# Optimization experiments

Hardware: AMD Instinct MI355X
Metric: run time of the kernel (lower is better)

Reference implementation:

```python
import jax, jax.numpy as jnp
import numpy as np

B, NV, JN = 1024, 8, 21
V = NV * JN            # 168 tokens = num_view * joint_num
F_DIM, NH, DQ, DV = 512, 4, 128, 128
HID = 512
EPS = 1e-6
NEG = float(-2**32 + 1)


def _layer_norm(x, g, b):
    mu = jnp.mean(x, axis=-1, keepdims=True)
    var = jnp.mean(jnp.square(x - mu), axis=-1, keepdims=True)
    return (x - mu) * jax.lax.rsqrt(var + EPS) * g + b


def setup_inputs() -> dict:
    key = jax.random.key(0)
    ks = jax.random.split(key, 12)
    s = 0.02
    return {
        "x": jax.random.normal(ks[0], (B, V, F_DIM), dtype=jnp.float32),
        "valid": jax.random.randint(ks[1], (B, NV), 0, 2),
        "wq": jax.random.normal(ks[2], (NH * DQ, F_DIM), dtype=jnp.float32) * s,
        "bq": jnp.zeros((NH * DQ,), dtype=jnp.float32),
        "wk": jax.random.normal(ks[3], (NH * DQ, F_DIM), dtype=jnp.float32) * s,
        "bk": jnp.zeros((NH * DQ,), dtype=jnp.float32),
        "wv": jax.random.normal(ks[4], (NH * DV, F_DIM), dtype=jnp.float32) * s,
        "bv": jnp.zeros((NH * DV,), dtype=jnp.float32),
        "fc_w": jax.random.normal(ks[5], (F_DIM, NH * DV), dtype=jnp.float32) * s,
        "fc_b": jnp.zeros((F_DIM,), dtype=jnp.float32),
        "ln1_g": jnp.ones((F_DIM,), dtype=jnp.float32),
        "ln1_b": jnp.zeros((F_DIM,), dtype=jnp.float32),
        "ln2_g": jnp.ones((F_DIM,), dtype=jnp.float32),
        "ln2_b": jnp.zeros((F_DIM,), dtype=jnp.float32),
        "fc1_w": jax.random.normal(ks[6], (HID, F_DIM), dtype=jnp.float32) * s,
        "fc1_b": jnp.zeros((HID,), dtype=jnp.float32),
        "fc2_w": jax.random.normal(ks[7], (F_DIM, HID), dtype=jnp.float32) * s,
        "fc2_b": jnp.zeros((F_DIM,), dtype=jnp.float32),
    }


def reference(x, valid, wq, bq, wk, bk, wv, bv, fc_w, fc_b,
              ln1_g, ln1_b, ln2_g, ln2_b, fc1_w, fc1_b, fc2_w, fc2_b):
    bs = x.shape[0]
    h = _layer_norm(x, ln1_g, ln1_b)                          # [B,V,f]
    q = (h @ wq.T + bq).reshape(bs, V, NH, DQ)                # [B,V,H,dq]
    k = (h @ wk.T + bk).reshape(bs, V, NH, DQ)
    v = (h @ wv.T + bv).reshape(bs, V, NH, DV)
    attn = jnp.einsum('bqhd,bkhd->bhqk', q, k) / jnp.sqrt(jnp.float32(DQ))
    # valid mask: per-view validity expanded to per-token, pairwise additive
    w = jnp.where(valid == 0, NEG, 0.0).astype(x.dtype)       # [B,NV]
    w = jnp.repeat(w, JN, axis=1)                             # [B,V], view-major
    m = w[:, :, None] + w[:, None, :]                         # [B,V,V]
    attn = attn + m[:, None, :, :]
    attn = jax.nn.softmax(attn, axis=-1)
    out = jnp.einsum('bhqk,bkhd->bqhd', attn, v).reshape(bs, V, NH * DV)
    out = out @ fc_w.T + fc_b
    x = x + out
    # MLP residual block
    h2 = _layer_norm(x, ln2_g, ln2_b)
    h2 = jax.nn.relu(h2 @ fc1_w.T + fc1_b) @ fc2_w.T + fc2_b
    return x + h2
```

## Files before the change

### kernel.cpp

```cpp
#include <hip/hip_runtime.h>
#include <stdint.h>

#define BATCH 1024
#define NVIEW 8
#define JN_   21
#define VTOK  168
#define FDIM  512
#define NHEAD 4
#define DHEAD 128
#define MROWS (BATCH*VTOK)
#define SCALE2 0.127517434f

typedef __attribute__((ext_vector_type(8))) short s8v;
typedef __attribute__((ext_vector_type(4))) short s4v;
typedef __attribute__((ext_vector_type(4))) float f4v;

static __device__ __forceinline__ short f2bf(float f){
  unsigned u = __builtin_bit_cast(unsigned, f);
  unsigned r = (u + 0x7FFFu + ((u >> 16) & 1u)) >> 16;
  return (short)(unsigned short)r;
}
static __device__ __forceinline__ float bf2f(short s){
  unsigned u = ((unsigned)(unsigned short)s) << 16;
  return __builtin_bit_cast(float, u);
}

#define GL16(gp, lp) __builtin_amdgcn_global_load_lds( \
    (__attribute__((address_space(1))) void*)(gp), \
    (__attribute__((address_space(3))) void*)(lp), 16, 0, 0)

__global__ __launch_bounds__(256) void convert_w(
    const float* __restrict__ wq, const float* __restrict__ wk,
    const float* __restrict__ wv, const float* __restrict__ fcw,
    const float* __restrict__ fc1, const float* __restrict__ fc2,
    short* __restrict__ dst){
  int id = blockIdx.x * 256 + threadIdx.x;
  int e = id * 4;
  int seg = e >> 18;
  int off = e & 262143;
  const float* s = seg==0?wq: seg==1?wk: seg==2?wv: seg==3?fcw: seg==4?fc1: fc2;
  float4 u = *(const float4*)(s + off);
  s4v o; o[0]=f2bf(u.x); o[1]=f2bf(u.y); o[2]=f2bf(u.z); o[3]=f2bf(u.w);
  *(s4v*)(dst + e) = o;
}

__global__ __launch_bounds__(256) void ln1_kernel(
    const float* __restrict__ x, const float* __restrict__ g,
    const float* __restrict__ bb, short* __restrict__ h){
  int row  = blockIdx.x * 4 + (threadIdx.x >> 6);
  int lane = threadIdx.x & 63;
  size_t base = (size_t)row * 512 + lane * 8;
  float4 u0 = *(const float4*)(x + base);
  float4 u1 = *(const float4*)(x + base + 4);
  float s = u0.x+u0.y+u0.z+u0.w + u1.x+u1.y+u1.z+u1.w;
  float q = u0.x*u0.x+u0.y*u0.y+u0.z*u0.z+u0.w*u0.w
          + u1.x*u1.x+u1.y*u1.y+u1.z*u1.z+u1.w*u1.w;
  #pragma unroll
  for (int o = 1; o < 64; o <<= 1){ s += __shfl_xor(s,o); q += __shfl_xor(q,o); }
  float mu = s * (1.f/512.f);
  float rstd = rsqrtf(q*(1.f/512.f) - mu*mu + 1e-6f);
  float4 g0 = *(const float4*)(g + lane*8),  g1 = *(const float4*)(g + lane*8 + 4);
  float4 b0 = *(const float4*)(bb + lane*8), b1 = *(const float4*)(bb + lane*8 + 4);
  s8v o_;
  o_[0]=f2bf((u0.x-mu)*rstd*g0.x+b0.x); o_[1]=f2bf((u0.y-mu)*rstd*g0.y+b0.y);
  o_[2]=f2bf((u0.z-mu)*rstd*g0.z+b0.z); o_[3]=f2bf((u0.w-mu)*rstd*g0.w+b0.w);
  o_[4]=f2bf((u1.x-mu)*rstd*g1.x+b1.x); o_[5]=f2bf((u1.y-mu)*rstd*g1.y+b1.y);
  o_[6]=f2bf((u1.z-mu)*rstd*g1.z+b1.z); o_[7]=f2bf((u1.w-mu)*rstd*g1.w+b1.w);
  *(s8v*)(h + base) = o_;
}

__global__ __launch_bounds__(256) void resid_ln(
    const float* __restrict__ x, const short* __restrict__ y,
    const float* __restrict__ g, const float* __restrict__ bb,
    short* __restrict__ x2b, short* __restrict__ g2){
  int row  = blockIdx.x * 4 + (threadIdx.x >> 6);
  int lane = threadIdx.x & 63;
  size_t base = (size_t)row * 512 + lane * 8;
  float4 u0 = *(const float4*)(x + base);
  float4 u1 = *(const float4*)(x + base + 4);
  s8v yv = *(const s8v*)(y + base);
  float v[8];
  v[0]=u0.x+bf2f(yv[0]); v[1]=u0.y+bf2f(yv[1]); v[2]=u0.z+bf2f(yv[2]); v[3]=u0.w+bf2f(yv[3]);
  v[4]=u1.x+bf2f(yv[4]); v[5]=u1.y+bf2f(yv[5]); v[6]=u1.z+bf2f(yv[6]); v[7]=u1.w+bf2f(yv[7]);
  s8v xv;
  #pragma unroll
  for (int i = 0; i < 8; i++) xv[i] = f2bf(v[i]);
  *(s8v*)(x2b + base) = xv;
  float s = 0.f, q = 0.f;
  #pragma unroll
  for (int i = 0; i < 8; i++){ s += v[i]; q += v[i]*v[i]; }
  #pragma unroll
  for (int o = 1; o < 64; o <<= 1){ s += __shfl_xor(s,o); q += __shfl_xor(q,o); }
  float mu = s * (1.f/512.f);
  float rstd = rsqrtf(q*(1.f/512.f) - mu*mu + 1e-6f);
  float4 g0 = *(const float4*)(g + lane*8),  g1 = *(const float4*)(g + lane*8 + 4);
  float4 b0 = *(const float4*)(bb + lane*8), b1 = *(const float4*)(bb + lane*8 + 4);
  s8v o_;
  o_[0]=f2bf((v[0]-mu)*rstd*g0.x+b0.x); o_[1]=f2bf((v[1]-mu)*rstd*g0.y+b0.y);
  o_[2]=f2bf((v[2]-mu)*rstd*g0.z+b0.z); o_[3]=f2bf((v[3]-mu)*rstd*g0.w+b0.w);
  o_[4]=f2bf((v[4]-mu)*rstd*g1.x+b1.x); o_[5]=f2bf((v[5]-mu)*rstd*g1.y+b1.y);
  o_[6]=f2bf((v[6]-mu)*rstd*g1.z+b1.z); o_[7]=f2bf((v[7]-mu)*rstd*g1.w+b1.w);
  *(s8v*)(g2 + base) = o_;
}

template<int MODE>
__global__ __launch_bounds__(512, 4) void gemm_bt(
    const short* __restrict__ A, const short* __restrict__ Bm,
    const float* __restrict__ bias0, const float* __restrict__ bias1,
    const short* __restrict__ aux, short* __restrict__ out0,
    short* __restrict__ out1, float* __restrict__ outf){
  __shared__ short lds[36864];
  short* const AL = lds;
  short* const BL = lds + 24576;
  const int tid = threadIdx.x, lane = tid & 63;
  const int wid = tid >> 6, wr = wid >> 1, wc = wid & 1;
  const int lg = lane >> 4, l15 = lane & 15;
  const int nwg  = gridDim.x * gridDim.y;
  const int flat = blockIdx.y * gridDim.x + blockIdx.x;
  const int swz  = (flat & 7) * (nwg >> 3) + (flat >> 3);
  size_t mt, nt;
  if (MODE == 1){ mt = swz & 1; nt = (size_t)(swz >> 1); }
  else {
    constexpr int GX = (MODE == 0) ? 8 : 4;
    nt = swz % GX; mt = swz / GX;
  }
  const size_t m0 = mt * 256, n0 = nt * 128;
  const short* Ab = A + m0 * 512;
  const short* Bb = Bm + n0 * 512;

#define STAGE_T(tt) do {                                                \
    short* da_ = AL + ((tt)%3)*8192;                                    \
    _Pragma("unroll")                                                   \
    for (int r_ = 0; r_ < 2; r_++){                                     \
      int c_ = r_*512 + tid;                                            \
      int row_ = c_ >> 2, chk_ = (c_ & 3) ^ (row_ & 3);                 \
      GL16(Ab + (size_t)row_*512 + (tt)*32 + chk_*8, da_ + c_*8);       \
    }                                                                   \
    {                                                                   \
      short* db_ = BL + ((tt)%3)*4096;                                  \
      int row_ = tid >> 2, chk_ = (tid & 3) ^ (row_ & 3);               \
      GL16(Bb + (size_t)row_*512 + (tt)*32 + chk_*8, db_ + tid*8);      \
    } } while(0)

  STAGE_T(0); STAGE_T(1);
  asm volatile("s_waitcnt vmcnt(3)" ::: "memory");
  __builtin_amdgcn_s_barrier();

  f4v acc[4][4];
  #pragma unroll
  for (int m=0;m<4;m++)
    #pragma unroll
    for (int n=0;n<4;n++) acc[m][n] = f4v{0.f,0.f,0.f,0.f};

  #pragma unroll
  for (int t = 0; t < 16; ++t){
    const short* Awp = AL + (t%3)*8192 + (wr*64 + l15)*32;
    const short* Bwp = BL + (t%3)*4096 + (wc*64 + l15)*32;
    const int cA = (lg ^ (l15 & 3)) * 8;
    s8v af[4], bf[4];
    #pragma unroll
    for (int m=0;m<4;m++) af[m] = *(const s8v*)(Awp + m*512 + cA);
    #pragma unroll
    for (int n=0;n<4;n++) bf[n] = *(const s8v*)(Bwp + n*512 + cA);
    if (t < 14) STAGE_T(t+2);
    __builtin_amdgcn_s_barrier();
    __builtin_amdgcn_s_setprio(1);
    #pragma unroll
    for (int m=0;m<4;m++)
      #pragma unroll
      for (int n=0;n<4;n++)
        acc[m][n] = __builtin_amdgcn_mfma_f32_16x16x32_bf16(af[m], bf[n], acc[m][n], 0,0,0);
    __builtin_amdgcn_s_setprio(0);
    if (t <= 13)      asm volatile("s_waitcnt vmcnt(3)" ::: "memory");
    else if (t == 14) asm volatile("s_waitcnt vmcnt(0)" ::: "memory");
    __builtin_amdgcn_s_barrier();
  }
#undef STAGE_T

  #pragma unroll
  for (int m=0;m<4;m++)
  #pragma unroll
  for (int n=0;n<4;n++)
  #pragma unroll
  for (int r=0;r<4;r++){
    int rowL = wr*64 + m*16 + lg*4 + r;
    int colL = wc*64 + n*16 + l15;
    size_t gm = m0 + rowL, gn = n0 + colL;
    float val = acc[m][n][r];
    if (MODE == 0){
      int nn = (int)gn;
      val += (nn < 512) ? bias0[nn] : bias1[nn - 512];
      int head = (nn >> 7) & 3, d = nn & 127;
      size_t b = gm / 168, tok = gm - b * 168;
      size_t idx = ((b*4 + head)*168 + tok)*128 + d;
      ((nn < 512) ? out0 : out1)[idx] = f2bf(val);
    } else if (MODE == 1){
      val += bias0[gm];
      int hh = ((int)gm >> 7) & 3, d = (int)gm & 127;
      size_t b = gn / 168, tok = gn - b * 168;
      out0[((b*4 + hh)*128 + d)*168 + tok] = f2bf(val);
    } else if (MODE == 2 || MODE == 3){
      val += bias0[gn];
      if (MODE == 3) val = fmaxf(val, 0.f);
      out0[gm*512 + gn] = f2bf(val);
    } else {
      val += bias0[gn] + bf2f(aux[gm*512 + gn]);
      outf[gm*512 + gn] = val;
    }
  }
}

__global__ __launch_bounds__(256, 2) void attn_kernel(
    const short* __restrict__ qg_, const short* __restrict__ kg_,
    const short* __restrict__ vtg_, const int* __restrict__ valid,
    short* __restrict__ outp){
  __shared__ short Ps[192*200];

  int tid = threadIdx.x, lane = tid & 63, wid = tid >> 6;
  int lg = lane >> 4, l15 = lane & 15;
  int bh = blockIdx.x, b = bh >> 2, hh = bh & 3;
  const short* qg  = qg_  + (size_t)bh * (168*128);
  const short* kg  = kg_  + (size_t)bh * (168*128);
  const short* vtg = vtg_ + (size_t)bh * (128*168);

  int bits = 0;
  #pragma unroll
  for (int v = 0; v < 8; v++) bits |= (valid[b*8 + v] != 0) << v;
  if (bits == 0) bits = 255;
  float wk2[11];
  #pragma unroll
  for (int n = 0; n < 11; n++){
    int kt = n*16 + l15;
    int view = (kt * 781) >> 14;
    wk2[n] = ((bits >> view) & 1) ? 0.0f : -1.0e9f;
  }

  int row0 = wid * 48;
  f4v zf = {0.f,0.f,0.f,0.f};

  s8v qf[3][4];
  #pragma unroll
  for (int m=0;m<3;m++)
    #pragma unroll
    for (int kf=0;kf<4;kf++)
      qf[m][kf] = *(const s8v*)(qg + (size_t)(row0 + m*16 + l15)*128 + kf*32 + lg*8);

  f4v accS[3][11];
  #pragma unroll
  for (int m=0;m<3;m++)
    #pragma unroll
    for (int n=0;n<11;n++) accS[m][n] = zf;
  s8v kb[3][4];
  #pragma unroll
  for (int p=0;p<2;p++)
    #pragma unroll
    for (int kf=0;kf<4;kf++)
      kb[p][kf] = *(const s8v*)(kg + (size_t)(p*16 + l15)*128 + kf*32 + lg*8);
  #pragma unroll
  for (int n=0;n<11;n++){
    if (n < 9){
      #pragma unroll
      for (int kf=0;kf<4;kf++)
        kb[(n+2)%3][kf] = *(const s8v*)(kg + (size_t)((n+2)*16 + l15)*128 + kf*32 + lg*8);
    }
    __builtin_amdgcn_s_setprio(1);
    #pragma unroll
    for (int kf=0;kf<4;kf++)
      #pragma unroll
      for (int m=0;m<3;m++)
        accS[m][n] = __builtin_amdgcn_mfma_f32_16x16x32_bf16(qf[m][kf], kb[n%3][kf], accS[m][n], 0,0,0);
    __builtin_amdgcn_s_setprio(0);
  }

  float inv_[3][4];
  #pragma unroll
  for (int m=0;m<3;m++){
    #pragma unroll
    for (int r=0;r<4;r++){
      int qtok = row0 + m*16 + lg*4 + r;
      float sum = 0.f;
      #pragma unroll
      for (int n=0;n<11;n++){
        float p = exp2f(fmaf(accS[m][n][r], SCALE2, wk2[n]));
        sum += p;
        Ps[qtok*200 + n*16 + l15] = f2bf(p);
      }
      sum += __shfl_xor(sum,1); sum += __shfl_xor(sum,2);
      sum += __shfl_xor(sum,4); sum += __shfl_xor(sum,8);
      inv_[m][r] = 1.0f / sum;
    }
  }
  {
    s8v z8 = {0,0,0,0,0,0,0,0};
    for (int i = lane; i < 96; i += 64){
      int rr = row0 + (i >> 1);
      *(s8v*)&Ps[rr*200 + 176 + (i&1)*8] = z8;
    }
  }

  s8v ap[3][6];
  #pragma unroll
  for (int m=0;m<3;m++)
    #pragma unroll
    for (int kf=0;kf<6;kf++)
      ap[m][kf] = *(const s8v*)&Ps[(row0 + m*16 + l15)*200 + kf*32 + lg*8];

  f4v accO[3][8];
  #pragma unroll
  for (int m=0;m<3;m++)
    #pragma unroll
    for (int n=0;n<8;n++) accO[m][n] = zf;
  s8v vb[3][6];
  #pragma unroll
  for (int p=0;p<2;p++)
    #pragma unroll
    for (int kf=0;kf<6;kf++)
      vb[p][kf] = *(const s8v*)(vtg + (size_t)(p*16 + l15)*168 + kf*32 + lg*8);
  #pragma unroll
  for (int n=0;n<8;n++){
    if (n < 6){
      #pragma unroll
      for (int kf=0;kf<6;kf++)
        vb[(n+2)%3][kf] = *(const s8v*)(vtg + (size_t)((n+2)*16 + l15)*168 + kf*32 + lg*8);
    }
    __builtin_amdgcn_s_setprio(1);
    #pragma unroll
    for (int kf=0;kf<6;kf++)
      #pragma unroll
      for (int m=0;m<3;m++)
        accO[m][n] = __builtin_amdgcn_mfma_f32_16x16x32_bf16(ap[m][kf], vb[n%3][kf], accO[m][n], 0,0,0);
    __builtin_amdgcn_s_setprio(0);
  }

  #pragma unroll
  for (int m=0;m<3;m++){
    #pragma unroll
    for (int r=0;r<4;r++){
      int qtok = row0 + m*16 + lg*4 + r;
      if (qtok < 168){
        float iv = inv_[m][r];
        size_t base = ((size_t)b*168 + qtok)*512 + hh*128;
        #pragma unroll
        for (int n=0;n<8;n++)
          outp[base + n*16 + l15] = f2bf(accO[m][n][r] * iv);
      }
    }
  }
}

extern "C" void kernel_launch(void* const* d_in, const int* in_sizes, int n_in,
                              void* d_out, int out_size, void* d_ws, size_t ws_size,
                              hipStream_t stream) {
  const float* x     = (const float*)d_in[0];
  const int*   valid = (const int*)  d_in[1];
  const float* wq    = (const float*)d_in[2];
  const float* bq    = (const float*)d_in[3];
  const float* wk    = (const float*)d_in[4];
  const float* bk    = (const float*)d_in[5];
  const float* wv    = (const float*)d_in[6];
  const float* bv    = (const float*)d_in[7];
  const float* fcw   = (const float*)d_in[8];
  const float* fcb   = (const float*)d_in[9];
  const float* ln1g  = (const float*)d_in[10];
  const float* ln1b  = (const float*)d_in[11];
  const float* ln2g  = (const float*)d_in[12];
  const float* ln2b  = (const float*)d_in[13];
  const float* fc1w  = (const float*)d_in[14];
  const float* fc1b  = (const float*)d_in[15];
  const float* fc2w  = (const float*)d_in[16];
  const float* fc2b  = (const float*)d_in[17];

  char* ws = (char*)d_ws;
  short* h       = (short*)(ws + 0LL);
  short* q_ws    = (short*)(ws + 176160768LL);
  short* k_ws    = (short*)(ws + 352321536LL);
  short* vt_ws   = (short*)(ws + 528482304LL);
  short* wb      = (short*)(ws + 704643072LL);
  short* attn_o  = h;
  short* y       = q_ws;
  short* g2      = h;
  short* a1      = k_ws;
  short* x2b     = vt_ws;
  float* outp    = (float*)d_out;

  convert_w<<<1536, 256, 0, stream>>>(wq, wk, wv, fcw, fc1w, fc2w, wb);
  ln1_kernel<<<MROWS/4, 256, 0, stream>>>(x, ln1g, ln1b, h);
  gemm_bt<0><<<dim3(8, MROWS/256), 512, 0, stream>>>(h, wb, bq, bk, nullptr, q_ws, k_ws, nullptr);
  gemm_bt<1><<<dim3(2, MROWS/128), 512, 0, stream>>>(wb + 524288, h, bv, nullptr, nullptr, vt_ws, nullptr, nullptr);
  attn_kernel<<<BATCH*NHEAD, 256, 0, stream>>>(q_ws, k_ws, vt_ws, valid, attn_o);
  gemm_bt<2><<<dim3(4, MROWS/256), 512, 0, stream>>>(attn_o, wb + 786432, fcb, nullptr, nullptr, y, nullptr, nullptr);
  resid_ln<<<MROWS/4, 256, 0, stream>>>(x, y, ln2g, ln2b, x2b, g2);
  gemm_bt<3><<<dim3(4, MROWS/256), 512, 0, stream>>>(g2, wb + 1048576, fc1b, nullptr, nullptr, a1, nullptr, nullptr);
  gemm_bt<4><<<dim3(4, MROWS/256), 512, 0, stream>>>(a1, wb + 1310720, fc2b, nullptr, x2b, nullptr, nullptr, outp);
}
```

Baseline: 1.346 ms.

## Retile GEMM to 128x128 blocks with 256 threads and 64-wide K steps

Shrinks the GEMM workgroup from 512 to 256 threads and the M tile from 256 to 128. K is now staged in 64-wide chunks with an 8-way XOR swizzle. A is triple-buffered and B double-buffered, with each half-K MFMA phase interleaved with the next stage's loads. The aim is to cut barrier counts per K and improve overlap and occupancy. In exchange each block re-reads B across more M tiles, which raises global traffic, and the new wait-count schedule is subtle.

```diff
diff --git a/kernel.cpp b/kernel.cpp
--- a/kernel.cpp
+++ b/kernel.cpp
@@ -104,46 +104,51 @@
 }
 
 template<int MODE>
-__global__ __launch_bounds__(512, 4) void gemm_bt(
+__global__ __launch_bounds__(256, 2) void gemm_bt(
     const short* __restrict__ A, const short* __restrict__ Bm,
     const float* __restrict__ bias0, const float* __restrict__ bias1,
     const short* __restrict__ aux, short* __restrict__ out0,
     short* __restrict__ out1, float* __restrict__ outf){
-  __shared__ short lds[36864];
+  __shared__ short lds[40960];
   short* const AL = lds;
   short* const BL = lds + 24576;
   const int tid = threadIdx.x, lane = tid & 63;
   const int wid = tid >> 6, wr = wid >> 1, wc = wid & 1;
-  const int lg = lane >> 4, l15 = lane & 15;
+  const int lg = lane >> 4, l15 = lane & 15, l7 = lane & 7;
   const int nwg  = gridDim.x * gridDim.y;
   const int flat = blockIdx.y * gridDim.x + blockIdx.x;
   const int swz  = (flat & 7) * (nwg >> 3) + (flat >> 3);
   size_t mt, nt;
-  if (MODE == 1){ mt = swz & 1; nt = (size_t)(swz >> 1); }
-  else {
-    constexpr int GX = (MODE == 0) ? 8 : 4;
-    nt = swz % GX; mt = swz / GX;
-  }
-  const size_t m0 = mt * 256, n0 = nt * 128;
+  if (MODE == 0)      { nt = swz & 7; mt = swz >> 3; }
+  else if (MODE == 1) { mt = swz & 3; nt = swz >> 2; }
+  else                { nt = swz & 3; mt = swz >> 2; }
+  const size_t m0 = mt * 128, n0 = nt * 128;
   const short* Ab = A + m0 * 512;
   const short* Bb = Bm + n0 * 512;
 
-#define STAGE_T(tt) do {                                                \
-    short* da_ = AL + ((tt)%3)*8192;                                    \
+#define STAGEA(tt) do {                                                 \
+    short* d_ = AL + ((tt)%3)*8192;                                     \
     _Pragma("unroll")                                                   \
-    for (int r_ = 0; r_ < 2; r_++){                                     \
-      int c_ = r_*512 + tid;                                            \
-      int row_ = c_ >> 2, chk_ = (c_ & 3) ^ (row_ & 3);                 \
-      GL16(Ab + (size_t)row_*512 + (tt)*32 + chk_*8, da_ + c_*8);       \
-    }                                                                   \
-    {                                                                   \
-      short* db_ = BL + ((tt)%3)*4096;                                  \
-      int row_ = tid >> 2, chk_ = (tid & 3) ^ (row_ & 3);               \
-      GL16(Bb + (size_t)row_*512 + (tt)*32 + chk_*8, db_ + tid*8);      \
+    for (int r_ = 0; r_ < 4; r_++){                                     \
+      int c_ = r_*256 + tid;                                            \
+      int row_ = c_ >> 3, chk_ = (c_ & 7) ^ (row_ & 7);                 \
+      GL16(Ab + (size_t)row_*512 + (tt)*64 + chk_*8, d_ + c_*8);        \
     } } while(0)
-
-  STAGE_T(0); STAGE_T(1);
-  asm volatile("s_waitcnt vmcnt(3)" ::: "memory");
+#define STAGEB(tt) do {                                                 \
+    short* d_ = BL + ((tt)%2)*8192;                                     \
+    _Pragma("unroll")                                                   \
+    for (int r_ = 0; r_ < 4; r_++){                                     \
+      int c_ = r_*256 + tid;                                            \
+      int row_ = c_ >> 3, chk_ = (c_ & 7) ^ (row_ & 7);                 \
+      GL16(Bb + (size_t)row_*512 + (tt)*64 + chk_*8, d_ + c_*8);        \
+    } } while(0)
+#define PWAIT() do {                                                    \
+    __builtin_amdgcn_s_barrier();                                       \
+    asm volatile("s_waitcnt lgkmcnt(0)" ::: "memory");                  \
+    __builtin_amdgcn_sched_barrier(0); } while(0)
+
+  STAGEA(0); STAGEB(0); STAGEA(1);
+  asm volatile("s_waitcnt vmcnt(4)" ::: "memory");
   __builtin_amdgcn_s_barrier();
 
   f4v acc[4][4];
@@ -152,18 +157,19 @@
     #pragma unroll
     for (int n=0;n<4;n++) acc[m][n] = f4v{0.f,0.f,0.f,0.f};
 
-  #pragma unroll
-  for (int t = 0; t < 16; ++t){
-    const short* Awp = AL + (t%3)*8192 + (wr*64 + l15)*32;
-    const short* Bwp = BL + (t%3)*4096 + (wc*64 + l15)*32;
-    const int cA = (lg ^ (l15 & 3)) * 8;
-    s8v af[4], bf[4];
-    #pragma unroll
-    for (int m=0;m<4;m++) af[m] = *(const s8v*)(Awp + m*512 + cA);
-    #pragma unroll
-    for (int n=0;n<4;n++) bf[n] = *(const s8v*)(Bwp + n*512 + cA);
-    if (t < 14) STAGE_T(t+2);
-    __builtin_amdgcn_s_barrier();
+  s8v af[4], bf[4];
+  #pragma unroll
+  for (int t = 0; t < 8; ++t){
+    const short* Awp = AL + (t%3)*8192 + (wr*64 + l15)*64;
+    const short* Bwp = BL + (t%2)*8192 + (wc*64 + l15)*64;
+    const int c0 = (lg ^ l7) * 8;
+    const int c1 = ((4 + lg) ^ l7) * 8;
+    #pragma unroll
+    for (int m=0;m<4;m++) af[m] = *(const s8v*)(Awp + m*1024 + c0);
+    #pragma unroll
+    for (int n=0;n<4;n++) bf[n] = *(const s8v*)(Bwp + n*1024 + c0);
+    if (t < 7) STAGEB(t+1);
+    PWAIT();
     __builtin_amdgcn_s_setprio(1);
     #pragma unroll
     for (int m=0;m<4;m++)
@@ -171,11 +177,27 @@
       for (int n=0;n<4;n++)
         acc[m][n] = __builtin_amdgcn_mfma_f32_16x16x32_bf16(af[m], bf[n], acc[m][n], 0,0,0);
     __builtin_amdgcn_s_setprio(0);
-    if (t <= 13)      asm volatile("s_waitcnt vmcnt(3)" ::: "memory");
-    else if (t == 14) asm volatile("s_waitcnt vmcnt(0)" ::: "memory");
     __builtin_amdgcn_s_barrier();
-  }
-#undef STAGE_T
+    #pragma unroll
+    for (int m=0;m<4;m++) af[m] = *(const s8v*)(Awp + m*1024 + c1);
+    #pragma unroll
+    for (int n=0;n<4;n++) bf[n] = *(const s8v*)(Bwp + n*1024 + c1);
+    if (t < 6) STAGEA(t+2);
+    PWAIT();
+    __builtin_amdgcn_s_setprio(1);
+    #pragma unroll
+    for (int m=0;m<4;m++)
+      #pragma unroll
+      for (int n=0;n<4;n++)
+        acc[m][n] = __builtin_amdgcn_mfma_f32_16x16x32_bf16(af[m], bf[n], acc[m][n], 0,0,0);
+    __builtin_amdgcn_s_setprio(0);
+    if (t < 6)       asm volatile("s_waitcnt vmcnt(4)" ::: "memory");
+    else if (t == 6) asm volatile("s_waitcnt vmcnt(0)" ::: "memory");
+    __builtin_amdgcn_s_barrier();
+  }
+#undef STAGEA
+#undef STAGEB
+#undef PWAIT
 
   #pragma unroll
   for (int m=0;m<4;m++)
@@ -385,11 +407,11 @@
 
   convert_w<<<1536, 256, 0, stream>>>(wq, wk, wv, fcw, fc1w, fc2w, wb);
   ln1_kernel<<<MROWS/4, 256, 0, stream>>>(x, ln1g, ln1b, h);
-  gemm_bt<0><<<dim3(8, MROWS/256), 512, 0, stream>>>(h, wb, bq, bk, nullptr, q_ws, k_ws, nullptr);
-  gemm_bt<1><<<dim3(2, MROWS/128), 512, 0, stream>>>(wb + 524288, h, bv, nullptr, nullptr, vt_ws, nullptr, nullptr);
+  gemm_bt<0><<<dim3(8, MROWS/128), 256, 0, stream>>>(h, wb, bq, bk, nullptr, q_ws, k_ws, nullptr);
+  gemm_bt<1><<<dim3(4, MROWS/128), 256, 0, stream>>>(wb + 524288, h, bv, nullptr, nullptr, vt_ws, nullptr, nullptr);
   attn_kernel<<<BATCH*NHEAD, 256, 0, stream>>>(q_ws, k_ws, vt_ws, valid, attn_o);
-  gemm_bt<2><<<dim3(4, MROWS/256), 512, 0, stream>>>(attn_o, wb + 786432, fcb, nullptr, nullptr, y, nullptr, nullptr);
+  gemm_bt<2><<<dim3(4, MROWS/128), 256, 0, stream>>>(attn_o, wb + 786432, fcb, nullptr, nullptr, y, nullptr, nullptr);
   resid_ln<<<MROWS/4, 256, 0, stream>>>(x, y, ln2g, ln2b, x2b, g2);
-  gemm_bt<3><<<dim3(4, MROWS/256), 512, 0, stream>>>(g2, wb + 1048576, fc1b, nullptr, nullptr, a1, nullptr, nullptr);
-  gemm_bt<4><<<dim3(4, MROWS/256), 512, 0, stream>>>(a1, wb + 1310720, fc2b, nullptr, x2b, nullptr, nullptr, outp);
-}
+  gemm_bt<3><<<dim3(4, MROWS/128), 256, 0, stream>>>(g2, wb + 1048576, fc1b, nullptr, nullptr, a1, nullptr, nullptr);
+  gemm_bt<4><<<dim3(4, MROWS/128), 256, 0, stream>>>(a1, wb + 1310720, fc2b, nullptr, x2b, nullptr, nullptr, outp);
+}
```

After: 1.357 ms. About the same (+0.8%).
